# Kernel optimization log

Hardware: AMD Instinct MI355X
Metric: run time of the kernel (lower is better)

The kernel has to match this reference:

```python
import jax, jax.numpy as jnp
import numpy as np

B, S, N, D, H = 16, 12, 400, 512, 8   # batch, in_steps, num_nodes, model_dim, num_heads
HD = D // H                            # head_dim = 64


def setup_inputs() -> dict:
    rng = jax.random.key(0)
    ks = jax.random.split(rng, 11)
    s = 0.02  # weight init scale
    return {
        "query": jax.random.normal(ks[0], (B, S, N, D), jnp.float32),
        "key":   jax.random.normal(ks[1], (B, S, N, D), jnp.float32),
        "value": jax.random.normal(ks[2], (B, S, N, D), jnp.float32),
        # nn.Linear weights are stored (out_features, in_features); applied as x @ W.T + b
        "Wq": jax.random.normal(ks[3], (D, D), jnp.float32) * s,
        "bq": jnp.zeros((D,), jnp.float32),
        "Wk": jax.random.normal(ks[4], (D, D), jnp.float32) * s,
        "bk": jnp.zeros((D,), jnp.float32),
        "Wv": jax.random.normal(ks[5], (D, D), jnp.float32) * s,
        "bv": jnp.zeros((D,), jnp.float32),
        "Wo": jax.random.normal(ks[6], (D, D), jnp.float32) * s,
        "bo": jnp.zeros((D,), jnp.float32),
    }


def reference(query, key, value, Wq, bq, Wk, bk, Wv, bv, Wo, bo):
    # Linear projections, then head split. torch's split(head_dim,-1)+cat(dim=0)
    # is equivalent to reshape(..., H, HD) with heads placed head-major on dim 0.
    q = (query @ Wq.T + bq).reshape(B, S, N, H, HD)
    k = (key   @ Wk.T + bk).reshape(B, S, N, H, HD)
    v = (value @ Wv.T + bv).reshape(B, S, N, H, HD)

    # attention across the node dim: scores (B, H, S, Nq, Nk)
    scores = jnp.einsum("bsqhd,bskhd->bhsqk", q, k) / jnp.float32(np.sqrt(HD))
    attn = jax.nn.softmax(scores, axis=-1)
    out = jnp.einsum("bhsqk,bskhd->bsqhd", attn, v).reshape(B, S, N, D)
    out = out @ Wo.T + bo

    # match torch's (H*B, S, N, N) / (H*B, S, N, HD) layouts for aux outputs
    scores_hb = scores.transpose(1, 0, 2, 3, 4).reshape(H * B, S, N, N)
    v_hb = v.transpose(3, 0, 1, 2, 4).reshape(H * B, S, N, HD)
    return out, scores_hb, v_hb
```

## Files before the change

### kernel.cpp

```cpp
#include <hip/hip_runtime.h>


typedef float fvec4 __attribute__((ext_vector_type(4)));
typedef float f32x4 __attribute__((ext_vector_type(4)));
typedef unsigned short usvec4 __attribute__((ext_vector_type(4)));
typedef unsigned short usvec8 __attribute__((ext_vector_type(8)));
typedef short v8s __attribute__((ext_vector_type(8)));

#define DEV __device__ __forceinline__

DEV unsigned short f2bf(float f) {
  unsigned int u = __builtin_bit_cast(unsigned int, f);
  u += 0x7FFFu + ((u >> 16) & 1u);
  return (unsigned short)(u >> 16);
}

DEV f32x4 mfma16(v8s a, v8s b, f32x4 c) {
  return __builtin_amdgcn_mfma_f32_16x16x32_bf16(a, b, c, 0, 0, 0);
}

DEV void gload16(const void* g, void* l) {
  __builtin_amdgcn_global_load_lds(
      (const __attribute__((address_space(1))) unsigned int*)g,
      (__attribute__((address_space(3))) unsigned int*)l, 16, 0, 0);
}

__global__ __launch_bounds__(256) void cvtw_k(const float* __restrict__ w0,
                                              const float* __restrict__ w1,
                                              const float* __restrict__ w2,
                                              const float* __restrict__ w3,
                                              unsigned short* __restrict__ o) {
  const float* w = (blockIdx.y == 0) ? w0 : (blockIdx.y == 1) ? w1
                 : (blockIdx.y == 2) ? w2 : w3;
  unsigned short* op = o + (long)blockIdx.y * 262144;
  long i = ((long)blockIdx.x * 256 + threadIdx.x) * 8;
  fvec4 a = *reinterpret_cast<const fvec4*>(w + i);
  fvec4 b = *reinterpret_cast<const fvec4*>(w + i + 4);
  usvec8 r;
  r[0] = f2bf(a[0]); r[1] = f2bf(a[1]); r[2] = f2bf(a[2]); r[3] = f2bf(a[3]);
  r[4] = f2bf(b[0]); r[5] = f2bf(b[1]); r[6] = f2bf(b[2]); r[7] = f2bf(b[3]);
  *reinterpret_cast<usvec8*>(op + i) = r;
}

__global__ __launch_bounds__(256) void proj_k(
    const float* __restrict__ qin, const float* __restrict__ kin,
    const float* __restrict__ vin, const unsigned short* __restrict__ wW,
    const float* __restrict__ bqp, const float* __restrict__ bkp,
    const float* __restrict__ bvp, unsigned short* __restrict__ wq_,
    unsigned short* __restrict__ wk_, float* __restrict__ vhb,
    unsigned short* __restrict__ wvt) {
  __shared__ unsigned short sMem[18432];
  const int t = threadIdx.x;
  const int lane = t & 63, wid = t >> 6;
  const int wm = wid >> 1, wn = wid & 1;
  const int lr = lane & 15, lg = lane >> 4;
  const int bid = blockIdx.x;
  const int orig = (bid & 7) * 900 + (bid >> 3);
  const int which = orig >= 4800 ? 2 : (orig >= 2400 ? 1 : 0);
  const int inner = orig - which * 2400;
  const long m0 = (long)(inner >> 2) * 128;
  const int n0 = (inner & 3) * 128;

  const float* A = which == 0 ? qin : which == 1 ? kin : vin;
  const unsigned short* W = wW + (long)which * 262144;
  const float* bias = which == 0 ? bqp : which == 1 ? bkp : bvp;

  const int srow = wid * 16 + (lane >> 2);
  const int scol = (lane & 3) * 8;
  const unsigned short* bS0 = W + (long)(n0 + srow) * 512 + scol;
  const unsigned short* bS1 = bS0 + 64 * 512;
  const int bOff0 = wid * 512;
  const int bOff1 = (wid + 4) * 512;

  const int arow = t >> 3;
  const int acol = (t & 7) * 4;
  const float* aP32 = A + (m0 + arow) * 512 + acol;
  const int aOff = arow * 40 + acol;

  f32x4 acc[4][4] = {};
  fvec4 aReg[4];
#pragma unroll
  for (int i = 0; i < 4; i++)
    aReg[i] = *reinterpret_cast<const fvec4*>(aP32 + (long)i * 16384);

  {
    unsigned short* sA0 = sMem;
    unsigned short* sB0 = sMem + 10240;
    gload16(bS0, sB0 + bOff0);
    gload16(bS1, sB0 + bOff1);
#pragma unroll
    for (int i = 0; i < 4; i++) {
      usvec4 pk;
      pk[0] = f2bf(aReg[i][0]); pk[1] = f2bf(aReg[i][1]);
      pk[2] = f2bf(aReg[i][2]); pk[3] = f2bf(aReg[i][3]);
      *reinterpret_cast<usvec4*>(sA0 + aOff + i * 1280) = pk;
    }
#pragma unroll
    for (int i = 0; i < 4; i++)
      aReg[i] = *reinterpret_cast<const fvec4*>(aP32 + (long)i * 16384 + 32);
  }
  __syncthreads();

  for (int k0 = 0; k0 < 512; k0 += 32) {
    const int c = (k0 >> 5) & 1;
    unsigned short* sAc = sMem + c * 5120;
    unsigned short* sBc = sMem + 10240 + c * 4096;
    if (k0 < 480) {
      unsigned short* sAn = sMem + (c ^ 1) * 5120;
      unsigned short* sBn = sMem + 10240 + (c ^ 1) * 4096;
      gload16(bS0 + k0 + 32, sBn + bOff0);
      gload16(bS1 + k0 + 32, sBn + bOff1);
#pragma unroll
      for (int i = 0; i < 4; i++) {
        usvec4 pk;
        pk[0] = f2bf(aReg[i][0]); pk[1] = f2bf(aReg[i][1]);
        pk[2] = f2bf(aReg[i][2]); pk[3] = f2bf(aReg[i][3]);
        *reinterpret_cast<usvec4*>(sAn + aOff + i * 1280) = pk;
      }
      if (k0 < 448) {
#pragma unroll
        for (int i = 0; i < 4; i++)
          aReg[i] = *reinterpret_cast<const fvec4*>(aP32 + (long)i * 16384 +
                                                    k0 + 64);
      }
    }

    v8s af[4], bf[4];
#pragma unroll
    for (int i = 0; i < 4; i++)
      af[i] = *reinterpret_cast<const v8s*>(&sAc[(wm * 64 + i * 16 + lr) * 40 + lg * 8]);
#pragma unroll
    for (int j = 0; j < 4; j++)
      bf[j] = *reinterpret_cast<const v8s*>(&sBc[(wn * 64 + j * 16 + lr) * 32 + lg * 8]);
    __builtin_amdgcn_s_setprio(1);
#pragma unroll
    for (int i = 0; i < 4; i++)
#pragma unroll
      for (int j = 0; j < 4; j++) acc[i][j] = mfma16(af[i], bf[j], acc[i][j]);
    __builtin_amdgcn_s_setprio(0);
    __syncthreads();
  }

  if (which <= 1) {
    unsigned short* o_h = which == 0 ? wq_ : wk_;
#pragma unroll
    for (int i = 0; i < 4; i++) {
#pragma unroll
      for (int j = 0; j < 4; j++) {
        const int col = wn * 64 + j * 16 + lr;
        const float bv_ = bias[n0 + col];
#pragma unroll
        for (int r = 0; r < 4; r++) {
          const int row = wm * 64 + i * 16 + lg * 4 + r;
          sMem[row * 140 + col] = f2bf(acc[i][j][r] + bv_);
        }
      }
    }
    __syncthreads();
#pragma unroll
    for (int pass = 0; pass < 2; pass++) {
      const int row = (t >> 2) + pass * 64;
      const int c0 = (t & 3) * 8;
      const unsigned short* src = &sMem[row * 140 + c0];
      unsigned short* dst = &o_h[(m0 + row) * 512 + n0 + c0];
#pragma unroll
      for (int k = 0; k < 4; k++)
        *reinterpret_cast<usvec8*>(dst + k * 32) =
            *reinterpret_cast<const usvec8*>(src + k * 32);
    }
  } else {
#pragma unroll
    for (int i = 0; i < 4; i++) {
#pragma unroll
      for (int j = 0; j < 4; j++) {
        const int gn = n0 + wn * 64 + j * 16 + lr;
        const float bv_ = bias[gn];
        const long gm0 = m0 + wm * 64 + i * 16 + lg * 4;
        const int bs_lin = (int)(gm0 / 400);
        const int node0 = (int)(gm0 - (long)bs_lin * 400);
        const int h = gn >> 6, hd = gn & 63;
        float* vp = vhb + ((((long)(h * 192 + bs_lin) * 400 + node0) << 6) + hd);
        const float v0 = acc[i][j][0] + bv_, v1 = acc[i][j][1] + bv_;
        const float v2 = acc[i][j][2] + bv_, v3 = acc[i][j][3] + bv_;
        vp[0] = v0;
        vp[64] = v1;
        vp[128] = v2;
        vp[192] = v3;
        usvec4 pk;
        pk[0] = f2bf(v0); pk[1] = f2bf(v1); pk[2] = f2bf(v2); pk[3] = f2bf(v3);
        *reinterpret_cast<usvec4*>(
            wvt + (((long)(bs_lin * 8 + h) * 64 + hd) * 400 + node0)) = pk;
      }
    }
  }
}

__global__ __launch_bounds__(256) void outgemm_k(
    const unsigned short* __restrict__ A, const unsigned short* __restrict__ W,
    const float* __restrict__ bias, float* __restrict__ o_f) {
  __shared__ unsigned short sMem[16384];
  const int t = threadIdx.x;
  const int lane = t & 63, wid = t >> 6;
  const int wm = wid >> 1, wn = wid & 1;
  const int lr = lane & 15, lg = lane >> 4;
  const int bid = blockIdx.x;
  const int orig = (bid & 7) * 300 + (bid >> 3);
  const long m0 = (long)(orig >> 2) * 128;
  const int n0 = (orig & 3) * 128;

  const int srow = wid * 16 + (lane >> 2);
  const int scol = (lane & 3) * 8;
  const unsigned short* aS0 = A + (m0 + srow) * 512 + scol;
  const unsigned short* aS1 = aS0 + 64 * 512;
  const unsigned short* bS0 = W + (long)(n0 + srow) * 512 + scol;
  const unsigned short* bS1 = bS0 + 64 * 512;
  const int bOff0 = wid * 512;
  const int bOff1 = (wid + 4) * 512;

  f32x4 acc[4][4] = {};

  {
    gload16(aS0, sMem + bOff0);
    gload16(aS1, sMem + bOff1);
    gload16(bS0, sMem + 8192 + bOff0);
    gload16(bS1, sMem + 8192 + bOff1);
  }
  __syncthreads();

  for (int k0 = 0; k0 < 512; k0 += 32) {
    const int c = (k0 >> 5) & 1;
    unsigned short* sAc = sMem + c * 4096;
    unsigned short* sBc = sMem + 8192 + c * 4096;
    if (k0 < 480) {
      unsigned short* sAn = sMem + (c ^ 1) * 4096;
      unsigned short* sBn = sMem + 8192 + (c ^ 1) * 4096;
      gload16(aS0 + k0 + 32, sAn + bOff0);
      gload16(aS1 + k0 + 32, sAn + bOff1);
      gload16(bS0 + k0 + 32, sBn + bOff0);
      gload16(bS1 + k0 + 32, sBn + bOff1);
    }

    v8s af[4], bf[4];
#pragma unroll
    for (int i = 0; i < 4; i++)
      af[i] = *reinterpret_cast<const v8s*>(&sAc[(wm * 64 + i * 16 + lr) * 32 + lg * 8]);
#pragma unroll
    for (int j = 0; j < 4; j++)
      bf[j] = *reinterpret_cast<const v8s*>(&sBc[(wn * 64 + j * 16 + lr) * 32 + lg * 8]);
    __builtin_amdgcn_s_setprio(1);
#pragma unroll
    for (int i = 0; i < 4; i++)
#pragma unroll
      for (int j = 0; j < 4; j++) acc[i][j] = mfma16(af[i], bf[j], acc[i][j]);
    __builtin_amdgcn_s_setprio(0);
    __syncthreads();
  }

#pragma unroll
  for (int i = 0; i < 4; i++) {
#pragma unroll
    for (int j = 0; j < 4; j++) {
      const int gn = n0 + wn * 64 + j * 16 + lr;
      const float bv_ = bias[gn];
#pragma unroll
      for (int r = 0; r < 4; r++) {
        const long gm = m0 + wm * 64 + i * 16 + lg * 4 + r;
        o_f[gm * 512 + gn] = acc[i][j][r] + bv_;
      }
    }
  }
}

__global__ __launch_bounds__(256) void attn_k(
    const unsigned short* __restrict__ qm, const unsigned short* __restrict__ km,
    const unsigned short* __restrict__ vt, float* __restrict__ sc,
    unsigned short* __restrict__ ctx) {
  __shared__ __align__(16) unsigned short sKV[25632];
  __shared__ __align__(16) unsigned short sP[32][424];
  __shared__ float redM[2][32], redS[2][32];
  const int t = threadIdx.x;
  const int lane = t & 63, wid = t >> 6;
  const int wq = wid >> 1, wk = wid & 1;
  const int lr = lane & 15, lg = lane >> 4;
  const int bid = blockIdx.x;
  const int orig = (bid & 7) * 2496 + (bid >> 3);
  const int g = orig / 13, qb = orig - g * 13;
  const int bs = g >> 3, h = g & 7;
  const int q0 = qb * 32;
  const long qkb = (long)bs * 204800 + h * 64;
  const long vtb = (long)g * 25600;

  {
    const unsigned short* kbase = km + qkb + (((lane & 7) ^ (lane >> 3)) << 3);
    for (int i = wid; i < 50; i += 4)
      gload16(kbase + (long)(i * 8 + (lane >> 3)) * 512, sKV + i * 512);
  }

  int qrow = q0 + wq * 16 + lr;
  if (qrow > 399) qrow = 399;
  const v8s aq0 = *reinterpret_cast<const v8s*>(qm + qkb + (long)qrow * 512 + lg * 8);
  const v8s aq1 = *reinterpret_cast<const v8s*>(qm + qkb + (long)qrow * 512 + 32 + lg * 8);

  __syncthreads();

  f32x4 acc[13];
#pragma unroll
  for (int f = 0; f < 13; f++) acc[f] = f32x4{0.f, 0.f, 0.f, 0.f};

#pragma unroll
  for (int f = 0; f < 13; f++) {
    int kr = wk * 208 + f * 16 + lr;
    if (kr > 399) kr = 399;
    const int sw = kr & 7;
    const v8s b0 = *reinterpret_cast<const v8s*>(sKV + kr * 64 + ((lg ^ sw) << 3));
    const v8s b1 = *reinterpret_cast<const v8s*>(sKV + kr * 64 + (((4 + lg) ^ sw) << 3));
    __builtin_amdgcn_s_setprio(1);
    acc[f] = mfma16(aq0, b0, acc[f]);
    acc[f] = mfma16(aq1, b1, acc[f]);
    __builtin_amdgcn_s_setprio(0);
  }

  const long sb = ((long)h * 192 + bs) * 160000;
  const int rowb = q0 + wq * 16 + lg * 4;
  const int rloc = wq * 16 + lg * 4;
  float mx[4] = {-3.0e38f, -3.0e38f, -3.0e38f, -3.0e38f};
#pragma unroll
  for (int f = 0; f < 13; f++) {
    const int col = wk * 208 + f * 16 + lr;
#pragma unroll
    for (int r = 0; r < 4; r++) {
      float s = acc[f][r] * 0.125f;
      if (col >= 400) s = -3.0e38f;
      acc[f][r] = s;
      mx[r] = fmaxf(mx[r], s);
      if (col < 400 && rowb + r < 400)
        sc[sb + (long)(rowb + r) * 400 + col] = s;
    }
  }
#pragma unroll
  for (int d = 1; d < 16; d <<= 1)
#pragma unroll
    for (int r = 0; r < 4; r++) mx[r] = fmaxf(mx[r], __shfl_xor(mx[r], d));
  if (lr == 0) {
#pragma unroll
    for (int r = 0; r < 4; r++) redM[wk][rloc + r] = mx[r];
  }
  __syncthreads();

  for (int i = wid; i < 50; i += 4)
    gload16(vt + vtb + i * 512 + lane * 8, sKV + i * 512);

  float M[4], sum[4] = {0.f, 0.f, 0.f, 0.f};
#pragma unroll
  for (int r = 0; r < 4; r++) M[r] = fmaxf(redM[0][rloc + r], redM[1][rloc + r]);
#pragma unroll
  for (int f = 0; f < 13; f++) {
#pragma unroll
    for (int r = 0; r < 4; r++) {
      float p = __expf(acc[f][r] - M[r]);
      sum[r] += p;
      sP[rloc + r][wk * 208 + f * 16 + lr] = f2bf(p);
    }
  }
#pragma unroll
  for (int d = 1; d < 16; d <<= 1)
#pragma unroll
    for (int r = 0; r < 4; r++) sum[r] += __shfl_xor(sum[r], d);
  if (lr == 0) {
#pragma unroll
    for (int r = 0; r < 4; r++) redS[wk][rloc + r] = sum[r];
  }
  __syncthreads();

  float inv[4];
#pragma unroll
  for (int r = 0; r < 4; r++) inv[r] = 1.0f / (redS[0][rloc + r] + redS[1][rloc + r]);

  const unsigned short* v0p = sKV + (wk * 32 + lr) * 400;
  const unsigned short* v1p = v0p + 6400;
  f32x4 o0 = {0.f, 0.f, 0.f, 0.f}, o1 = {0.f, 0.f, 0.f, 0.f};
#pragma unroll
  for (int ks = 0; ks < 13; ks++) {
    const v8s pa = *reinterpret_cast<const v8s*>(&sP[wq * 16 + lr][ks * 32 + lg * 8]);
    const v8s bv0 = *reinterpret_cast<const v8s*>(v0p + ks * 32 + lg * 8);
    const v8s bv1 = *reinterpret_cast<const v8s*>(v1p + ks * 32 + lg * 8);
    __builtin_amdgcn_s_setprio(1);
    o0 = mfma16(pa, bv0, o0);
    o1 = mfma16(pa, bv1, o1);
    __builtin_amdgcn_s_setprio(0);
  }

  const long cb = (long)bs * 400 * 512 + h * 64 + wk * 32;
#pragma unroll
  for (int r = 0; r < 4; r++) {
    const int row = rowb + r;
    if (row < 400) {
      ctx[cb + (long)row * 512 + lr] = f2bf(o0[r] * inv[r]);
      ctx[cb + (long)row * 512 + 16 + lr] = f2bf(o1[r] * inv[r]);
    }
  }
}


extern "C" void kernel_launch(void* const* d_in, const int* in_sizes, int n_in,
                              void* d_out, int out_size, void* d_ws, size_t ws_size,
                              hipStream_t stream) {
  (void)in_sizes; (void)n_in; (void)out_size;

  const float* query = (const float*)d_in[0];
  const float* key   = (const float*)d_in[1];
  const float* value = (const float*)d_in[2];
  const float* Wq = (const float*)d_in[3];
  const float* bq = (const float*)d_in[4];
  const float* Wk = (const float*)d_in[5];
  const float* bk = (const float*)d_in[6];
  const float* Wv = (const float*)d_in[7];
  const float* bv = (const float*)d_in[8];
  const float* Wo = (const float*)d_in[9];
  const float* bo = (const float*)d_in[10];

  float* out = (float*)d_out;
  float* sc  = out + 39321600ULL;
  float* vhb = sc + 245760000ULL;

  char* ws = (char*)d_ws;
  unsigned short* wq_  = (unsigned short*)ws;
  unsigned short* wk_  = (unsigned short*)(ws + 78643200ULL);
  unsigned short* wvt  = (unsigned short*)(ws + 157286400ULL);
  unsigned short* wW   = (unsigned short*)(ws + 235929600ULL);
  unsigned short* wctx = (ws_size >= 316669952ULL)
                             ? (unsigned short*)(ws + 238026752ULL)
                             : wq_;

  dim3 blk(256);

  hipLaunchKernelGGL(cvtw_k, dim3(128, 4), blk, 0, stream, Wq, Wk, Wv, Wo, wW);

  hipLaunchKernelGGL(proj_k, dim3(7200), blk, 0, stream, query, key, value, wW,
                     bq, bk, bv, wq_, wk_, vhb, wvt);

  hipLaunchKernelGGL(attn_k, dim3(19968), blk, 0, stream, wq_, wk_, wvt, sc, wctx);

  hipLaunchKernelGGL(outgemm_k, dim3(2400), blk, 0, stream, wctx, wW + 786432,
                     bo, out);
}
```

Measured before the change: 915.6 us.

## Process a whole (batch,step,head) group per block to load K/V once

The attention kernel now launches one 512-thread block per (batch·step, head) group instead of 13 blocks of 32 query rows. K and V are loaded into separate LDS buffers once, and the block then loops over 7 tiles of 64 query rows. This is meant to remove the repeated K/V global/L2 traffic across the 13 blocks that used to share each group. In exchange, LDS use per block rises to about 156 KB, which likely allows only one block per CU. It also loses the overlap of the V load with the softmax and adds some wasted padded query rows (448 vs 416).

```diff
diff --git a/kernel.cpp b/kernel.cpp
--- a/kernel.cpp
+++ b/kernel.cpp
@@ -271,132 +271,139 @@
   }
 }
 
-__global__ __launch_bounds__(256) void attn_k(
+__global__ __launch_bounds__(512) void attn_k(
     const unsigned short* __restrict__ qm, const unsigned short* __restrict__ km,
     const unsigned short* __restrict__ vt, float* __restrict__ sc,
     unsigned short* __restrict__ ctx) {
-  __shared__ __align__(16) unsigned short sKV[25632];
-  __shared__ __align__(16) unsigned short sP[32][424];
-  __shared__ float redM[2][32], redS[2][32];
+  __shared__ __align__(16) unsigned short sK[25600];
+  __shared__ __align__(16) unsigned short sV[25632];
+  __shared__ __align__(16) unsigned short sP[64][424];
+  __shared__ float redM[2][64], redS[2][64];
   const int t = threadIdx.x;
   const int lane = t & 63, wid = t >> 6;
   const int wq = wid >> 1, wk = wid & 1;
   const int lr = lane & 15, lg = lane >> 4;
-  const int bid = blockIdx.x;
-  const int orig = (bid & 7) * 2496 + (bid >> 3);
-  const int g = orig / 13, qb = orig - g * 13;
+  const int g = blockIdx.x;
   const int bs = g >> 3, h = g & 7;
-  const int q0 = qb * 32;
   const long qkb = (long)bs * 204800 + h * 64;
   const long vtb = (long)g * 25600;
 
   {
     const unsigned short* kbase = km + qkb + (((lane & 7) ^ (lane >> 3)) << 3);
-    for (int i = wid; i < 50; i += 4)
-      gload16(kbase + (long)(i * 8 + (lane >> 3)) * 512, sKV + i * 512);
-  }
-
-  int qrow = q0 + wq * 16 + lr;
-  if (qrow > 399) qrow = 399;
-  const v8s aq0 = *reinterpret_cast<const v8s*>(qm + qkb + (long)qrow * 512 + lg * 8);
-  const v8s aq1 = *reinterpret_cast<const v8s*>(qm + qkb + (long)qrow * 512 + 32 + lg * 8);
+    for (int i = wid; i < 50; i += 8)
+      gload16(kbase + (long)(i * 8 + (lane >> 3)) * 512, sK + i * 512);
+  }
+  for (int i = wid; i < 50; i += 8)
+    gload16(vt + vtb + i * 512 + lane * 8, sV + i * 512);
 
   __syncthreads();
 
-  f32x4 acc[13];
-#pragma unroll
-  for (int f = 0; f < 13; f++) acc[f] = f32x4{0.f, 0.f, 0.f, 0.f};
-
-#pragma unroll
-  for (int f = 0; f < 13; f++) {
-    int kr = wk * 208 + f * 16 + lr;
-    if (kr > 399) kr = 399;
-    const int sw = kr & 7;
-    const v8s b0 = *reinterpret_cast<const v8s*>(sKV + kr * 64 + ((lg ^ sw) << 3));
-    const v8s b1 = *reinterpret_cast<const v8s*>(sKV + kr * 64 + (((4 + lg) ^ sw) << 3));
-    __builtin_amdgcn_s_setprio(1);
-    acc[f] = mfma16(aq0, b0, acc[f]);
-    acc[f] = mfma16(aq1, b1, acc[f]);
-    __builtin_amdgcn_s_setprio(0);
-  }
-
   const long sb = ((long)h * 192 + bs) * 160000;
-  const int rowb = q0 + wq * 16 + lg * 4;
-  const int rloc = wq * 16 + lg * 4;
-  float mx[4] = {-3.0e38f, -3.0e38f, -3.0e38f, -3.0e38f};
-#pragma unroll
-  for (int f = 0; f < 13; f++) {
-    const int col = wk * 208 + f * 16 + lr;
+  const unsigned short* v0p = sV + (wk * 32 + lr) * 400;
+  const unsigned short* v1p = v0p + 6400;
+  const long cb = (long)bs * 400 * 512 + h * 64 + wk * 32;
+
+  for (int qt = 0; qt < 7; ++qt) {
+    const int q0 = qt * 64;
+    int qrow = q0 + wq * 16 + lr;
+    if (qrow > 399) qrow = 399;
+    const v8s aq0 =
+        *reinterpret_cast<const v8s*>(qm + qkb + (long)qrow * 512 + lg * 8);
+    const v8s aq1 =
+        *reinterpret_cast<const v8s*>(qm + qkb + (long)qrow * 512 + 32 + lg * 8);
+
+    f32x4 acc[13];
+#pragma unroll
+    for (int f = 0; f < 13; f++) acc[f] = f32x4{0.f, 0.f, 0.f, 0.f};
+
+#pragma unroll
+    for (int f = 0; f < 13; f++) {
+      int kr = wk * 208 + f * 16 + lr;
+      if (kr > 399) kr = 399;
+      const int sw = kr & 7;
+      const v8s b0 = *reinterpret_cast<const v8s*>(sK + kr * 64 + ((lg ^ sw) << 3));
+      const v8s b1 =
+          *reinterpret_cast<const v8s*>(sK + kr * 64 + (((4 + lg) ^ sw) << 3));
+      __builtin_amdgcn_s_setprio(1);
+      acc[f] = mfma16(aq0, b0, acc[f]);
+      acc[f] = mfma16(aq1, b1, acc[f]);
+      __builtin_amdgcn_s_setprio(0);
+    }
+
+    const int rowb = q0 + wq * 16 + lg * 4;
+    const int rloc = wq * 16 + lg * 4;
+    float mx[4] = {-3.0e38f, -3.0e38f, -3.0e38f, -3.0e38f};
+#pragma unroll
+    for (int f = 0; f < 13; f++) {
+      const int col = wk * 208 + f * 16 + lr;
+#pragma unroll
+      for (int r = 0; r < 4; r++) {
+        float s = acc[f][r] * 0.125f;
+        if (col >= 400) s = -3.0e38f;
+        acc[f][r] = s;
+        mx[r] = fmaxf(mx[r], s);
+        if (col < 400 && rowb + r < 400)
+          sc[sb + (long)(rowb + r) * 400 + col] = s;
+      }
+    }
+#pragma unroll
+    for (int d = 1; d < 16; d <<= 1)
+#pragma unroll
+      for (int r = 0; r < 4; r++) mx[r] = fmaxf(mx[r], __shfl_xor(mx[r], d));
+    if (lr == 0) {
+#pragma unroll
+      for (int r = 0; r < 4; r++) redM[wk][rloc + r] = mx[r];
+    }
+    __syncthreads();
+
+    float M[4], sum[4] = {0.f, 0.f, 0.f, 0.f};
+#pragma unroll
+    for (int r = 0; r < 4; r++)
+      M[r] = fmaxf(redM[0][rloc + r], redM[1][rloc + r]);
+#pragma unroll
+    for (int f = 0; f < 13; f++) {
+#pragma unroll
+      for (int r = 0; r < 4; r++) {
+        float p = __expf(acc[f][r] - M[r]);
+        sum[r] += p;
+        sP[rloc + r][wk * 208 + f * 16 + lr] = f2bf(p);
+      }
+    }
+#pragma unroll
+    for (int d = 1; d < 16; d <<= 1)
+#pragma unroll
+      for (int r = 0; r < 4; r++) sum[r] += __shfl_xor(sum[r], d);
+    if (lr == 0) {
+#pragma unroll
+      for (int r = 0; r < 4; r++) redS[wk][rloc + r] = sum[r];
+    }
+    __syncthreads();
+
+    float inv[4];
+#pragma unroll
+    for (int r = 0; r < 4; r++)
+      inv[r] = 1.0f / (redS[0][rloc + r] + redS[1][rloc + r]);
+
+    f32x4 o0 = {0.f, 0.f, 0.f, 0.f}, o1 = {0.f, 0.f, 0.f, 0.f};
+#pragma unroll
+    for (int ks = 0; ks < 13; ks++) {
+      const v8s pa =
+          *reinterpret_cast<const v8s*>(&sP[wq * 16 + lr][ks * 32 + lg * 8]);
+      const v8s bv0 = *reinterpret_cast<const v8s*>(v0p + ks * 32 + lg * 8);
+      const v8s bv1 = *reinterpret_cast<const v8s*>(v1p + ks * 32 + lg * 8);
+      __builtin_amdgcn_s_setprio(1);
+      o0 = mfma16(pa, bv0, o0);
+      o1 = mfma16(pa, bv1, o1);
+      __builtin_amdgcn_s_setprio(0);
+    }
+
 #pragma unroll
     for (int r = 0; r < 4; r++) {
-      float s = acc[f][r] * 0.125f;
-      if (col >= 400) s = -3.0e38f;
-      acc[f][r] = s;
-      mx[r] = fmaxf(mx[r], s);
-      if (col < 400 && rowb + r < 400)
-        sc[sb + (long)(rowb + r) * 400 + col] = s;
-    }
-  }
-#pragma unroll
-  for (int d = 1; d < 16; d <<= 1)
-#pragma unroll
-    for (int r = 0; r < 4; r++) mx[r] = fmaxf(mx[r], __shfl_xor(mx[r], d));
-  if (lr == 0) {
-#pragma unroll
-    for (int r = 0; r < 4; r++) redM[wk][rloc + r] = mx[r];
-  }
-  __syncthreads();
-
-  for (int i = wid; i < 50; i += 4)
-    gload16(vt + vtb + i * 512 + lane * 8, sKV + i * 512);
-
-  float M[4], sum[4] = {0.f, 0.f, 0.f, 0.f};
-#pragma unroll
-  for (int r = 0; r < 4; r++) M[r] = fmaxf(redM[0][rloc + r], redM[1][rloc + r]);
-#pragma unroll
-  for (int f = 0; f < 13; f++) {
-#pragma unroll
-    for (int r = 0; r < 4; r++) {
-      float p = __expf(acc[f][r] - M[r]);
-      sum[r] += p;
-      sP[rloc + r][wk * 208 + f * 16 + lr] = f2bf(p);
-    }
-  }
-#pragma unroll
-  for (int d = 1; d < 16; d <<= 1)
-#pragma unroll
-    for (int r = 0; r < 4; r++) sum[r] += __shfl_xor(sum[r], d);
-  if (lr == 0) {
-#pragma unroll
-    for (int r = 0; r < 4; r++) redS[wk][rloc + r] = sum[r];
-  }
-  __syncthreads();
-
-  float inv[4];
-#pragma unroll
-  for (int r = 0; r < 4; r++) inv[r] = 1.0f / (redS[0][rloc + r] + redS[1][rloc + r]);
-
-  const unsigned short* v0p = sKV + (wk * 32 + lr) * 400;
-  const unsigned short* v1p = v0p + 6400;
-  f32x4 o0 = {0.f, 0.f, 0.f, 0.f}, o1 = {0.f, 0.f, 0.f, 0.f};
-#pragma unroll
-  for (int ks = 0; ks < 13; ks++) {
-    const v8s pa = *reinterpret_cast<const v8s*>(&sP[wq * 16 + lr][ks * 32 + lg * 8]);
-    const v8s bv0 = *reinterpret_cast<const v8s*>(v0p + ks * 32 + lg * 8);
-    const v8s bv1 = *reinterpret_cast<const v8s*>(v1p + ks * 32 + lg * 8);
-    __builtin_amdgcn_s_setprio(1);
-    o0 = mfma16(pa, bv0, o0);
-    o1 = mfma16(pa, bv1, o1);
-    __builtin_amdgcn_s_setprio(0);
-  }
-
-  const long cb = (long)bs * 400 * 512 + h * 64 + wk * 32;
-#pragma unroll
-  for (int r = 0; r < 4; r++) {
-    const int row = rowb + r;
-    if (row < 400) {
-      ctx[cb + (long)row * 512 + lr] = f2bf(o0[r] * inv[r]);
-      ctx[cb + (long)row * 512 + 16 + lr] = f2bf(o1[r] * inv[r]);
+      const int row = rowb + r;
+      if (row < 400) {
+        ctx[cb + (long)row * 512 + lr] = f2bf(o0[r] * inv[r]);
+        ctx[cb + (long)row * 512 + 16 + lr] = f2bf(o1[r] * inv[r]);
+      }
     }
   }
 }
@@ -439,7 +446,8 @@
   hipLaunchKernelGGL(proj_k, dim3(7200), blk, 0, stream, query, key, value, wW,
                      bq, bk, bv, wq_, wk_, vhb, wvt);
 
-  hipLaunchKernelGGL(attn_k, dim3(19968), blk, 0, stream, wq_, wk_, wvt, sc, wctx);
+  hipLaunchKernelGGL(attn_k, dim3(1536), dim3(512), 0, stream, wq_, wk_, wvt,
+                     sc, wctx);
 
   hipLaunchKernelGGL(outgemm_k, dim3(2400), blk, 0, stream, wctx, wW + 786432,
                      bo, out);
```

Result: faster. 797.1 us (-12.9%).
